# Kernel tuning notes

Measured on AMD Instinct MI355X. Metric: run time of the kernel, lower is better.

The kernel has to match this reference:

```python
import jax, jax.numpy as jnp
import numpy as np

B, T_Q, T_KV, D = 4, 2048, 4096, 1024
H = 16
HD = D // H  # head_dim = 64
EPS_LN = 1e-5
EPS_NORM = 1e-12


def setup_inputs() -> dict:
    key = jax.random.key(0)
    ks = jax.random.split(key, 12)
    inp = {
        'query': jax.random.normal(ks[0], (B, T_Q, D), jnp.float32),
        'key':   jax.random.normal(ks[1], (B, T_KV, D), jnp.float32),
        'value': jax.random.normal(ks[2], (B, T_KV, D), jnp.float32),
        # projections (nn.Linear stores weight as [out, in]; y = x @ W.T)
        'Wq': jax.random.normal(ks[3], (D, D), jnp.float32) * 0.02,
        'Wk': jax.random.normal(ks[4], (D, D), jnp.float32) * 0.02,
        'Wv': jax.random.normal(ks[5], (D, D), jnp.float32) * 0.02,
        'Wo': jax.random.normal(ks[6], (D, D), jnp.float32) * 0.01,
        'bo': jnp.zeros((D,), jnp.float32),
        'Wbeta':  jax.random.normal(ks[7], (H, D), jnp.float32) * 0.02,
        'bbeta':  jnp.zeros((H,), jnp.float32),
        'Walpha': jax.random.normal(ks[8], (H, D), jnp.float32) * 0.02,
        'balpha': jnp.full((H,), -1.0, jnp.float32),
        # per-head-dim LayerNorms
        'gq': jnp.ones((HD,), jnp.float32),
        'bq': jnp.zeros((HD,), jnp.float32),
        'gk': jnp.ones((HD,), jnp.float32),
        'bk': jnp.zeros((HD,), jnp.float32),
    }
    return inp


def _layernorm(x, g, b):
    mu = jnp.mean(x, axis=-1, keepdims=True)
    var = jnp.mean(jnp.square(x - mu), axis=-1, keepdims=True)
    return (x - mu) * jax.lax.rsqrt(var + EPS_LN) * g + b


def reference(query, key, value, Wq, Wk, Wv, Wo, bo,
              Wbeta, bbeta, Walpha, balpha, gq, bq, gk, bk):
    Bq, Tq, Dm = query.shape
    Tkv = key.shape[1]

    q = (query @ Wq.T).reshape(Bq, Tq, H, HD)
    k = (key   @ Wk.T).reshape(Bq, Tkv, H, HD)
    v = (value @ Wv.T).reshape(Bq, Tkv, H, HD)

    q = _layernorm(q, gq, bq)
    k = _layernorm(k, gk, bk)
    # F.normalize(k, dim=-1)
    k = k / jnp.maximum(jnp.linalg.norm(k, axis=-1, keepdims=True), EPS_NORM)

    beta  = jax.nn.sigmoid(key @ Wbeta.T  + bbeta)   # [B, Tkv, H]
    alpha = jax.nn.sigmoid(key @ Walpha.T + balpha)  # [B, Tkv, H]

    # time-major for scan: [Tkv, B, H, ...]
    k_t = jnp.moveaxis(k, 1, 0)
    v_t = jnp.moveaxis(v, 1, 0)
    b_t = jnp.moveaxis(beta, 1, 0)
    a_t = jnp.moveaxis(alpha, 1, 0)

    M0 = jnp.zeros((Bq, H, HD, HD), query.dtype)

    def step(M, inputs):
        kt, vt, bt, at = inputs  # [B,H,d],[B,H,d],[B,H],[B,H]
        Mk = jnp.einsum('bhij,bhj->bhi', M, kt)
        erase = at[..., None, None] * jnp.einsum('bhi,bhj->bhij', Mk, kt)
        write = bt[..., None, None] * jnp.einsum('bhi,bhj->bhij', vt, kt)
        return M - erase + write, None

    M, _ = jax.lax.scan(step, M0, (k_t, v_t, b_t, a_t))

    # out[b,t,h,i] = sum_j M[b,h,i,j] * q[b,t,h,j]
    out = jnp.einsum('bhij,bthj->bthi', M, q).reshape(Bq, Tq, Dm)
    out = out @ Wo.T + bo  # dropout is identity in eval mode
    return out
```

## Files before the change

### kernel.cpp

```cpp
#include <hip/hip_runtime.h>
#include <math.h>

#define TQ_LEN 2048
#define TKV_LEN 4096
#define BATCH 4
#define DMODEL 1024
#define NH 16
#define HD 64
#define NKBA 1152
#define CCH 128
#define NCHUNK (TKV_LEN / CCH)

typedef unsigned short u16;
typedef __attribute__((ext_vector_type(8))) short bf16x8;
typedef __attribute__((ext_vector_type(4))) float f32x4;

__device__ __forceinline__ u16 f2bf(float x) {
  union { float f; unsigned u; } c; c.f = x;
  unsigned r = c.u + 0x7fffu + ((c.u >> 16) & 1u);
  return (u16)(r >> 16);
}
__device__ __forceinline__ float bf2f(u16 x) {
  union { unsigned u; float f; } c; c.u = ((unsigned)x) << 16;
  return c.f;
}

__device__ __forceinline__ float wave_sum64(float x) {
#pragma unroll
  for (int off = 32; off; off >>= 1) x += __shfl_xor(x, off, 64);
  return x;
}

__global__ __launch_bounds__(256) void cvt_bf16_kernel(
    const float* __restrict__ s, u16* __restrict__ d) {
  size_t i = ((size_t)blockIdx.x * 256 + threadIdx.x) * 8;
  float4 a = *(const float4*)&s[i];
  float4 b = *(const float4*)&s[i + 4];
  union { u16 h[8]; uint4 v; } o;
  o.h[0] = f2bf(a.x); o.h[1] = f2bf(a.y); o.h[2] = f2bf(a.z); o.h[3] = f2bf(a.w);
  o.h[4] = f2bf(b.x); o.h[5] = f2bf(b.y); o.h[6] = f2bf(b.z); o.h[7] = f2bf(b.w);
  *(uint4*)&d[i] = o.v;
}

__global__ __launch_bounds__(256) void wcat_bf_kernel(
    const float* __restrict__ Wk, const float* __restrict__ Wb,
    const float* __restrict__ Wa, u16* __restrict__ Wcat) {
  int i = blockIdx.x * 256 + threadIdx.x;
  int row = i / DMODEL, col = i % DMODEL;
  float v;
  if (row < 1024)      v = Wk[i];
  else if (row < 1040) v = Wb[(row - 1024) * DMODEL + col];
  else if (row < 1056) v = Wa[(row - 1040) * DMODEL + col];
  else                 v = 0.f;
  Wcat[i] = f2bf(v);
}

__device__ __forceinline__ void stage_tile_bf16(
    const u16* __restrict__ G, int ldg, int row0, int kcol0,
    u16* lds, int wid, int lane) {
#pragma unroll
  for (int e = 0; e < 2; ++e) {
    int r = (wid * 2 + e) * 16;
    const u16* g = G + (size_t)(row0 + r + (lane >> 2)) * ldg + kcol0 + (lane & 3) * 8;
    __builtin_amdgcn_global_load_lds(
        (const __attribute__((address_space(1))) void*)g,
        (__attribute__((address_space(3))) void*)(lds + r * 32), 16, 0, 0);
  }
}

template <bool HAS_BIAS, bool OUT_BF16>
__global__ __launch_bounds__(256) void gemm_bt_bf16(
    const u16* __restrict__ A, const u16* __restrict__ B,
    const float* __restrict__ bias, void* __restrict__ Cv,
    int M, int N, int K, int ldc) {
  __shared__ u16 Al[2][128 * 32];
  __shared__ u16 Bl[2][128 * 32];
  const int tid = threadIdx.x;
  const int wid = tid >> 6, lane = tid & 63;
  const int wr = wid >> 1, wc = wid & 1;
  const int bm = blockIdx.y * 128, bn = blockIdx.x * 128;
  const int lrow = lane & 15, lk = (lane >> 4) * 8;

  int aoff[4], boff[4];
#pragma unroll
  for (int f = 0; f < 4; ++f) {
    aoff[f] = (wr * 64 + f * 16 + lrow) * 32 + lk;
    boff[f] = (wc * 64 + f * 16 + lrow) * 32 + lk;
  }

  f32x4 acc[4][4] = {};
  const int nk = K >> 5;
  int cur = 0;
  stage_tile_bf16(A, K, bm, 0, &Al[0][0], wid, lane);
  stage_tile_bf16(B, K, bn, 0, &Bl[0][0], wid, lane);
  __syncthreads();
  for (int kt = 0; kt < nk; ++kt) {
    if (kt + 1 < nk) {
      stage_tile_bf16(A, K, bm, (kt + 1) * 32, &Al[cur ^ 1][0], wid, lane);
      stage_tile_bf16(B, K, bn, (kt + 1) * 32, &Bl[cur ^ 1][0], wid, lane);
    }
    bf16x8 af[4], bfr[4];
#pragma unroll
    for (int f = 0; f < 4; ++f) af[f] = *(const bf16x8*)&Al[cur][aoff[f]];
#pragma unroll
    for (int f = 0; f < 4; ++f) bfr[f] = *(const bf16x8*)&Bl[cur][boff[f]];
#pragma unroll
    for (int mf = 0; mf < 4; ++mf)
#pragma unroll
      for (int nf = 0; nf < 4; ++nf)
        acc[mf][nf] = __builtin_amdgcn_mfma_f32_16x16x32_bf16(
            af[mf], bfr[nf], acc[mf][nf], 0, 0, 0);
    __syncthreads();
    cur ^= 1;
  }
  const int crow0 = bm + wr * 64 + (lane >> 4) * 4;
  const int ccol0 = bn + wc * 64 + (lane & 15);
#pragma unroll
  for (int mf = 0; mf < 4; ++mf)
#pragma unroll
    for (int nf = 0; nf < 4; ++nf) {
      int col = ccol0 + nf * 16;
      float bv = HAS_BIAS ? bias[col] : 0.f;
#pragma unroll
      for (int i = 0; i < 4; ++i) {
        int row = crow0 + mf * 16 + i;
        float vout = acc[mf][nf][i] + bv;
        if (OUT_BF16)
          ((u16*)Cv)[(size_t)row * ldc + col] = f2bf(vout);
        else
          ((float*)Cv)[(size_t)row * ldc + col] = vout;
      }
    }
}

__global__ __launch_bounds__(256) void ln_q_kernel(float* __restrict__ q,
                                                   const float* __restrict__ g,
                                                   const float* __restrict__ b) {
  int gidx = blockIdx.x * 4 + (threadIdx.x >> 6);
  int lane = threadIdx.x & 63;
  int row = gidx >> 4, h = gidx & 15;
  float* p = q + (size_t)row * DMODEL + h * HD + lane;
  float x = *p;
  float mu = wave_sum64(x) * (1.f / 64.f);
  float d = x - mu;
  float var = wave_sum64(d * d) * (1.f / 64.f);
  float y = d * rsqrtf(var + 1e-5f) * g[lane] + b[lane];
  *p = y;
}

__global__ __launch_bounds__(256) void ln_k_kernel(float* __restrict__ kb,
                                                   const float* __restrict__ g,
                                                   const float* __restrict__ b) {
  int gidx = blockIdx.x * 4 + (threadIdx.x >> 6);
  int lane = threadIdx.x & 63;
  int row = gidx >> 4, h = gidx & 15;
  float* p = kb + (size_t)row * NKBA + h * HD + lane;
  float x = *p;
  float mu = wave_sum64(x) * (1.f / 64.f);
  float d = x - mu;
  float var = wave_sum64(d * d) * (1.f / 64.f);
  float y = d * rsqrtf(var + 1e-5f) * g[lane] + b[lane];
  float s2 = wave_sum64(y * y);
  y = y / fmaxf(sqrtf(s2), 1e-12f);
  *p = y;
}

__global__ __launch_bounds__(256) void sig_kernel(
    const float* __restrict__ kb, const float* __restrict__ bb,
    const float* __restrict__ ba, float* __restrict__ beta,
    float* __restrict__ alpha) {
  int i = blockIdx.x * 256 + threadIdx.x;
  int row = i >> 4, h = i & 15;
  float lb = kb[(size_t)row * NKBA + 1024 + h] + bb[h];
  float la = kb[(size_t)row * NKBA + 1040 + h] + ba[h];
  beta[i]  = 1.f / (1.f + expf(-lb));
  alpha[i] = 1.f / (1.f + expf(-la));
}

__global__ __launch_bounds__(64, 2) void chunk_scan_kernel(
    const float* __restrict__ kb, const u16* __restrict__ v,
    const float* __restrict__ beta, const float* __restrict__ alpha,
    float* __restrict__ Pbuf, float* __restrict__ Sbuf) {
  __shared__ float klds[2][64];
  int slot = blockIdx.x;
  int bh = slot / NCHUNK, ck = slot % NCHUNK;
  int b = bh >> 4, h = bh & 15;
  int lane = threadIdx.x;
  int t0 = ck * CCH;
  const float* kbase = kb + ((size_t)b * TKV_LEN + t0) * NKBA + h * HD;
  const u16* vbase = v + ((size_t)b * TKV_LEN + t0) * DMODEL + h * HD;
  const float* bbase = beta + ((size_t)b * TKV_LEN + t0) * NH + h;
  const float* abase = alpha + ((size_t)b * TKV_LEN + t0) * NH + h;

  float P[64], S[64];
#pragma unroll
  for (int j = 0; j < 64; ++j) { P[j] = (j == lane) ? 1.f : 0.f; S[j] = 0.f; }

  klds[0][lane] = kbase[lane];
  float kn = kbase[(size_t)NKBA + lane];
  float vn = bf2f(vbase[lane]);
  float btn = bbase[0];
  float atn = abase[0];

  for (int t = 0; t < CCH; ++t) {
    float vc = vn, bt = btn, at = atn;
    if (t + 1 < CCH) {
      vn = bf2f(vbase[(size_t)(t + 1) * DMODEL + lane]);
      btn = bbase[(size_t)(t + 1) * NH];
      atn = abase[(size_t)(t + 1) * NH];
    }
    klds[(t + 1) & 1][lane] = kn;
    kn = (t + 2 < CCH) ? kbase[(size_t)(t + 2) * NKBA + lane] : 0.f;
    const float* kcur = klds[t & 1];
    float pk0 = 0.f, pk1 = 0.f, sk0 = 0.f, sk1 = 0.f;
#pragma unroll
    for (int g = 0; g < 4; ++g) {
      float4 ka = *(const float4*)&kcur[g * 16 + 0];
      float4 kc = *(const float4*)&kcur[g * 16 + 4];
      float4 ke = *(const float4*)&kcur[g * 16 + 8];
      float4 kg = *(const float4*)&kcur[g * 16 + 12];
      pk0 = fmaf(P[g*16+ 0], ka.x, pk0); pk1 = fmaf(P[g*16+ 1], ka.y, pk1);
      pk0 = fmaf(P[g*16+ 2], ka.z, pk0); pk1 = fmaf(P[g*16+ 3], ka.w, pk1);
      pk0 = fmaf(P[g*16+ 4], kc.x, pk0); pk1 = fmaf(P[g*16+ 5], kc.y, pk1);
      pk0 = fmaf(P[g*16+ 6], kc.z, pk0); pk1 = fmaf(P[g*16+ 7], kc.w, pk1);
      pk0 = fmaf(P[g*16+ 8], ke.x, pk0); pk1 = fmaf(P[g*16+ 9], ke.y, pk1);
      pk0 = fmaf(P[g*16+10], ke.z, pk0); pk1 = fmaf(P[g*16+11], ke.w, pk1);
      pk0 = fmaf(P[g*16+12], kg.x, pk0); pk1 = fmaf(P[g*16+13], kg.y, pk1);
      pk0 = fmaf(P[g*16+14], kg.z, pk0); pk1 = fmaf(P[g*16+15], kg.w, pk1);
      sk0 = fmaf(S[g*16+ 0], ka.x, sk0); sk1 = fmaf(S[g*16+ 1], ka.y, sk1);
      sk0 = fmaf(S[g*16+ 2], ka.z, sk0); sk1 = fmaf(S[g*16+ 3], ka.w, sk1);
      sk0 = fmaf(S[g*16+ 4], kc.x, sk0); sk1 = fmaf(S[g*16+ 5], kc.y, sk1);
      sk0 = fmaf(S[g*16+ 6], kc.z, sk0); sk1 = fmaf(S[g*16+ 7], kc.w, sk1);
      sk0 = fmaf(S[g*16+ 8], ke.x, sk0); sk1 = fmaf(S[g*16+ 9], ke.y, sk1);
      sk0 = fmaf(S[g*16+10], ke.z, sk0); sk1 = fmaf(S[g*16+11], ke.w, sk1);
      sk0 = fmaf(S[g*16+12], kg.x, sk0); sk1 = fmaf(S[g*16+13], kg.y, sk1);
      sk0 = fmaf(S[g*16+14], kg.z, sk0); sk1 = fmaf(S[g*16+15], kg.w, sk1);
    }
    float cp = -at * (pk0 + pk1);
    float cs = fmaf(bt, vc, -at * (sk0 + sk1));
#pragma unroll
    for (int g = 0; g < 4; ++g) {
      float4 ka = *(const float4*)&kcur[g * 16 + 0];
      float4 kc = *(const float4*)&kcur[g * 16 + 4];
      float4 ke = *(const float4*)&kcur[g * 16 + 8];
      float4 kg = *(const float4*)&kcur[g * 16 + 12];
      P[g*16+ 0] = fmaf(cp, ka.x, P[g*16+ 0]); P[g*16+ 1] = fmaf(cp, ka.y, P[g*16+ 1]);
      P[g*16+ 2] = fmaf(cp, ka.z, P[g*16+ 2]); P[g*16+ 3] = fmaf(cp, ka.w, P[g*16+ 3]);
      P[g*16+ 4] = fmaf(cp, kc.x, P[g*16+ 4]); P[g*16+ 5] = fmaf(cp, kc.y, P[g*16+ 5]);
      P[g*16+ 6] = fmaf(cp, kc.z, P[g*16+ 6]); P[g*16+ 7] = fmaf(cp, kc.w, P[g*16+ 7]);
      P[g*16+ 8] = fmaf(cp, ke.x, P[g*16+ 8]); P[g*16+ 9] = fmaf(cp, ke.y, P[g*16+ 9]);
      P[g*16+10] = fmaf(cp, ke.z, P[g*16+10]); P[g*16+11] = fmaf(cp, ke.w, P[g*16+11]);
      P[g*16+12] = fmaf(cp, kg.x, P[g*16+12]); P[g*16+13] = fmaf(cp, kg.y, P[g*16+13]);
      P[g*16+14] = fmaf(cp, kg.z, P[g*16+14]); P[g*16+15] = fmaf(cp, kg.w, P[g*16+15]);
      S[g*16+ 0] = fmaf(cs, ka.x, S[g*16+ 0]); S[g*16+ 1] = fmaf(cs, ka.y, S[g*16+ 1]);
      S[g*16+ 2] = fmaf(cs, ka.z, S[g*16+ 2]); S[g*16+ 3] = fmaf(cs, ka.w, S[g*16+ 3]);
      S[g*16+ 4] = fmaf(cs, kc.x, S[g*16+ 4]); S[g*16+ 5] = fmaf(cs, kc.y, S[g*16+ 5]);
      S[g*16+ 6] = fmaf(cs, kc.z, S[g*16+ 6]); S[g*16+ 7] = fmaf(cs, kc.w, S[g*16+ 7]);
      S[g*16+ 8] = fmaf(cs, ke.x, S[g*16+ 8]); S[g*16+ 9] = fmaf(cs, ke.y, S[g*16+ 9]);
      S[g*16+10] = fmaf(cs, ke.z, S[g*16+10]); S[g*16+11] = fmaf(cs, ke.w, S[g*16+11]);
      S[g*16+12] = fmaf(cs, kg.x, S[g*16+12]); S[g*16+13] = fmaf(cs, kg.y, S[g*16+13]);
      S[g*16+14] = fmaf(cs, kg.z, S[g*16+14]); S[g*16+15] = fmaf(cs, kg.w, S[g*16+15]);
    }
  }
  float* po = Pbuf + (size_t)slot * 4096 + (size_t)lane * 64;
  float* so = Sbuf + (size_t)slot * 4096 + (size_t)lane * 64;
#pragma unroll
  for (int j4 = 0; j4 < 16; ++j4) {
    *(float4*)&po[j4 * 4] = make_float4(P[4 * j4], P[4 * j4 + 1], P[4 * j4 + 2], P[4 * j4 + 3]);
    *(float4*)&so[j4 * 4] = make_float4(S[4 * j4], S[4 * j4 + 1], S[4 * j4 + 2], S[4 * j4 + 3]);
  }
}

__global__ __launch_bounds__(256) void fold_kernel(
    const float* __restrict__ Pin, const float* __restrict__ Sin,
    float* __restrict__ Pout, float* __restrict__ Sout, int nitems) {
  __shared__ float Pa[64][68], Sa[64][68], Pc[64][68], Sc[64][68];
  const int tid = threadIdx.x;
  const int r0 = (tid >> 4) * 4, c0 = (tid & 15) * 4;
  for (int l = tid; l < 4096; l += 256) {
    int r = l >> 6, c = l & 63;
    Pa[r][c] = (r == c) ? 1.f : 0.f;
    Sa[r][c] = 0.f;
  }
  for (int item = 0; item < nitems; ++item) {
    const float* pg = Pin + ((size_t)blockIdx.x * nitems + item) * 4096;
    const float* sg = Sin + ((size_t)blockIdx.x * nitems + item) * 4096;
#pragma unroll
    for (int e = 0; e < 4; ++e) {
      int l = tid * 16 + e * 4;
      int r = l >> 6, c = l & 63;
      *(float4*)&Pc[r][c] = *(const float4*)&pg[l];
      *(float4*)&Sc[r][c] = *(const float4*)&sg[l];
    }
    __syncthreads();
    float accP[4][4] = {}, accS[4][4] = {};
#pragma unroll 4
    for (int j4 = 0; j4 < 16; ++j4) {
      float bmat[4][4];
#pragma unroll
      for (int jj = 0; jj < 4; ++jj) {
        float4 t = *(const float4*)&Pc[j4 * 4 + jj][c0];
        bmat[jj][0] = t.x; bmat[jj][1] = t.y; bmat[jj][2] = t.z; bmat[jj][3] = t.w;
      }
#pragma unroll
      for (int rr = 0; rr < 4; ++rr) {
        float4 tp = *(const float4*)&Pa[r0 + rr][j4 * 4];
        float4 ts = *(const float4*)&Sa[r0 + rr][j4 * 4];
        float ap[4] = {tp.x, tp.y, tp.z, tp.w};
        float as[4] = {ts.x, ts.y, ts.z, ts.w};
#pragma unroll
        for (int jj = 0; jj < 4; ++jj)
#pragma unroll
          for (int cc = 0; cc < 4; ++cc) {
            accP[rr][cc] = fmaf(ap[jj], bmat[jj][cc], accP[rr][cc]);
            accS[rr][cc] = fmaf(as[jj], bmat[jj][cc], accS[rr][cc]);
          }
      }
    }
#pragma unroll
    for (int rr = 0; rr < 4; ++rr)
#pragma unroll
      for (int cc = 0; cc < 4; ++cc) accS[rr][cc] += Sc[r0 + rr][c0 + cc];
    __syncthreads();
#pragma unroll
    for (int rr = 0; rr < 4; ++rr)
#pragma unroll
      for (int cc = 0; cc < 4; ++cc) {
        Pa[r0 + rr][c0 + cc] = accP[rr][cc];
        Sa[r0 + rr][c0 + cc] = accS[rr][cc];
      }
  }
  __syncthreads();
  float* po = Pout + (size_t)blockIdx.x * 4096;
  float* so = Sout + (size_t)blockIdx.x * 4096;
#pragma unroll
  for (int e = 0; e < 4; ++e) {
    int l = tid * 16 + e * 4;
    int r = l >> 6, c = l & 63;
    *(float4*)&po[l] = *(const float4*)&Pa[r][c];
    *(float4*)&so[l] = *(const float4*)&Sa[r][c];
  }
}

__global__ __launch_bounds__(256) void outm_kernel(
    const float* __restrict__ Mg, const float* __restrict__ q,
    u16* __restrict__ attn) {
  __shared__ float Ml[64][65];
  int bh = blockIdx.x;
  int tchunk = blockIdx.y;
  int b = bh >> 4, h = bh & 15;
  int tid = threadIdx.x;
  const float* mg = Mg + (size_t)bh * 4096;
#pragma unroll
  for (int e = 0; e < 16; ++e) {
    int l = tid + e * 256;
    Ml[l >> 6][l & 63] = mg[l];
  }
  __syncthreads();
  int lane = tid & 63, tt = tid >> 6;
  const float* qb = q + ((size_t)b * TQ_LEN + tchunk * 256) * DMODEL + h * HD;
  u16* ob = attn + ((size_t)b * TQ_LEN + tchunk * 256) * DMODEL + h * HD;
  for (int it = 0; it < 64; ++it) {
    int t = it * 4 + tt;
    const float* qr = qb + (size_t)t * DMODEL;
    float acc = 0.f;
#pragma unroll
    for (int j4 = 0; j4 < 16; ++j4) {
      float4 qv = *(const float4*)&qr[j4 * 4];
      acc += Ml[lane][j4 * 4 + 0] * qv.x + Ml[lane][j4 * 4 + 1] * qv.y +
             Ml[lane][j4 * 4 + 2] * qv.z + Ml[lane][j4 * 4 + 3] * qv.w;
    }
    ob[(size_t)t * DMODEL + lane] = f2bf(acc);
  }
}

extern "C" void kernel_launch(void* const* d_in, const int* in_sizes, int n_in,
                              void* d_out, int out_size, void* d_ws,
                              size_t ws_size, hipStream_t stream) {
  const float* query = (const float*)d_in[0];
  const float* key   = (const float*)d_in[1];
  const float* value = (const float*)d_in[2];
  const float* Wq    = (const float*)d_in[3];
  const float* Wk    = (const float*)d_in[4];
  const float* Wv    = (const float*)d_in[5];
  const float* Wo    = (const float*)d_in[6];
  const float* bo    = (const float*)d_in[7];
  const float* Wbeta = (const float*)d_in[8];
  const float* bbeta = (const float*)d_in[9];
  const float* Walpha= (const float*)d_in[10];
  const float* balpha= (const float*)d_in[11];
  const float* gq    = (const float*)d_in[12];
  const float* bq    = (const float*)d_in[13];
  const float* gk    = (const float*)d_in[14];
  const float* bk    = (const float*)d_in[15];
  float* out = (float*)d_out;

  const int MQ = BATCH * TQ_LEN;
  const int MKV = BATCH * TKV_LEN;
  const int NSLOT = 64 * NCHUNK;

  float* ws = (float*)d_ws;
  size_t off = 0;
  u16* Wcat_bf = (u16*)(ws + off); off += (size_t)NKBA * DMODEL / 2;
  u16* Wq_bf   = (u16*)(ws + off); off += (size_t)DMODEL * DMODEL / 2;
  u16* Wv_bf   = (u16*)(ws + off); off += (size_t)DMODEL * DMODEL / 2;
  u16* Wo_bf   = (u16*)(ws + off); off += (size_t)DMODEL * DMODEL / 2;
  u16* qbf = (u16*)(ws + off); size_t qbf_f = off; off += (size_t)MQ * DMODEL / 2;
  u16* kbf = (u16*)(ws + off); size_t kbf_f = off; off += (size_t)MKV * DMODEL / 2;
  u16* vbf = (u16*)(ws + off); size_t vbf_f = off; off += (size_t)MKV * DMODEL / 2;
  float* qp   = ws + off; off += (size_t)MQ * DMODEL;
  float* kba  = ws + off; size_t kba_f = off; off += (size_t)MKV * NKBA;
  u16* vpb = (u16*)(ws + off); off += (size_t)MKV * DMODEL / 2;
  float* Pbuf = ws + kbf_f;
  float* Sbuf = ws + vbf_f;
  float* Gp   = ws + qbf_f;
  float* Gs   = ws + qbf_f + 1048576;
  float* Fp   = ws + qbf_f + 2097152;
  float* beta = ws + qbf_f + 2359296;
  float* alpha= ws + qbf_f + 2621440;
  float* Mg   = ws + qbf_f + 2883584;
  u16* attn_bf = (u16*)(ws + kba_f);

  wcat_bf_kernel<<<NKBA * DMODEL / 256, 256, 0, stream>>>(Wk, Wbeta, Walpha, Wcat_bf);
  cvt_bf16_kernel<<<DMODEL * DMODEL / 2048, 256, 0, stream>>>(Wq, Wq_bf);
  cvt_bf16_kernel<<<DMODEL * DMODEL / 2048, 256, 0, stream>>>(Wv, Wv_bf);
  cvt_bf16_kernel<<<DMODEL * DMODEL / 2048, 256, 0, stream>>>(Wo, Wo_bf);
  cvt_bf16_kernel<<<MQ * DMODEL / 2048, 256, 0, stream>>>(query, qbf);
  cvt_bf16_kernel<<<MKV * DMODEL / 2048, 256, 0, stream>>>(key, kbf);
  cvt_bf16_kernel<<<MKV * DMODEL / 2048, 256, 0, stream>>>(value, vbf);
  gemm_bt_bf16<false, false><<<dim3(DMODEL / 128, MQ / 128), 256, 0, stream>>>(
      qbf, Wq_bf, nullptr, qp, MQ, DMODEL, DMODEL, DMODEL);
  gemm_bt_bf16<false, false><<<dim3(NKBA / 128, MKV / 128), 256, 0, stream>>>(
      kbf, Wcat_bf, nullptr, kba, MKV, NKBA, DMODEL, NKBA);
  gemm_bt_bf16<false, true><<<dim3(DMODEL / 128, MKV / 128), 256, 0, stream>>>(
      vbf, Wv_bf, nullptr, vpb, MKV, DMODEL, DMODEL, DMODEL);
  ln_q_kernel<<<MQ * NH / 4, 256, 0, stream>>>(qp, gq, bq);
  ln_k_kernel<<<MKV * NH / 4, 256, 0, stream>>>(kba, gk, bk);
  sig_kernel<<<MKV * NH / 256, 256, 0, stream>>>(kba, bbeta, balpha, beta, alpha);
  chunk_scan_kernel<<<NSLOT, 64, 0, stream>>>(kba, vpb, beta, alpha, Pbuf, Sbuf);
  fold_kernel<<<NSLOT / 8, 256, 0, stream>>>(Pbuf, Sbuf, Gp, Gs, 8);
  fold_kernel<<<64, 256, 0, stream>>>(Gp, Gs, Fp, Mg, 4);
  outm_kernel<<<dim3(64, TQ_LEN / 256), 256, 0, stream>>>(Mg, qp, attn_bf);
  gemm_bt_bf16<true, false><<<dim3(DMODEL / 128, MQ / 128), 256, 0, stream>>>(
      attn_bf, Wo_bf, bo, out, MQ, DMODEL, DMODEL, DMODEL);
  (void)in_sizes; (void)n_in; (void)out_size; (void)ws_size;
}
```

Measured before the change: 606.6 us.

## Replace 128x128 GEMM with 256x256 tile, 8-wave ping-pong pipelined GEMM

Swaps the 128x128, K=32 double-buffered bf16 GEMM for a 256x256, K=64 tile kernel with 512 threads. The new kernel interleaves global-to-LDS staging with MFMA phases using explicit barriers, wave priority and vmcnt waits, and adds an XCD-aware block swizzle. NKBA is padded to 1280 so the concatenated K/beta/alpha projection divides into 256-wide tiles. The aim is more data reuse per LDS byte and better overlap of memory with compute, at the cost of 128 KB of LDS, fewer blocks (smaller grids), and some wasted compute on the padded columns.

```diff
diff --git a/kernel.cpp b/kernel.cpp
--- a/kernel.cpp
+++ b/kernel.cpp
@@ -7,7 +7,7 @@
 #define DMODEL 1024
 #define NH 16
 #define HD 64
-#define NKBA 1152
+#define NKBA 1280
 #define CCH 128
 #define NCHUNK (TKV_LEN / CCH)
 
@@ -55,82 +55,138 @@
   Wcat[i] = f2bf(v);
 }
 
-__device__ __forceinline__ void stage_tile_bf16(
-    const u16* __restrict__ G, int ldg, int row0, int kcol0,
-    u16* lds, int wid, int lane) {
+#define BAR() __builtin_amdgcn_s_barrier()
+#define PRIO(x) __builtin_amdgcn_s_setprio(x)
+#define VMCNT(n)                                              \
+  do {                                                        \
+    __builtin_amdgcn_sched_barrier(0);                        \
+    asm volatile("s_waitcnt vmcnt(" #n ")" ::: "memory");     \
+  } while (0)
+
+__device__ __forceinline__ void stage_half256(
+    const u16* __restrict__ G, int ldg, int row0, int kc, int h,
+    u16* ldsmat, int wid, int lane) {
 #pragma unroll
   for (int e = 0; e < 2; ++e) {
-    int r = (wid * 2 + e) * 16;
-    const u16* g = G + (size_t)(row0 + r + (lane >> 2)) * ldg + kcol0 + (lane & 3) * 8;
+    int j0 = wid * 64 + e * 512;
+    int j = j0 + lane;
+    int r = h * 128 + (j >> 3);
+    int cg = (j & 7) * 8;
+    const u16* g = G + (size_t)(row0 + r) * ldg + kc + cg;
     __builtin_amdgcn_global_load_lds(
         (const __attribute__((address_space(1))) void*)g,
-        (__attribute__((address_space(3))) void*)(lds + r * 32), 16, 0, 0);
-  }
-}
+        (__attribute__((address_space(3))) void*)(ldsmat + h * 8192 + j0 * 8),
+        16, 0, 0);
+  }
+}
+
+#define READ_A(L, h_)                                                         \
+  do {                                                                        \
+    _Pragma("unroll") for (int mf = 0; mf < 4; ++mf)                          \
+    _Pragma("unroll") for (int kk = 0; kk < 2; ++kk)                          \
+      af[mf][kk] = *(const bf16x8*)&(L)[(wm * 128 + (h_) * 64 + mf * 16 +     \
+                                         lrow) * 64 + kk * 32 + lk8];         \
+  } while (0)
+
+#define READ_B(L, n_, dst)                                                    \
+  do {                                                                        \
+    _Pragma("unroll") for (int nf = 0; nf < 2; ++nf)                          \
+    _Pragma("unroll") for (int kk = 0; kk < 2; ++kk)                          \
+      dst[nf][kk] = *(const bf16x8*)&(L)[(wn * 64 + (n_) * 32 + nf * 16 +     \
+                                          lrow) * 64 + kk * 32 + lk8];        \
+  } while (0)
+
+#define MFMA_Q(h_, n_, bfx)                                                   \
+  do {                                                                        \
+    _Pragma("unroll") for (int mf = 0; mf < 4; ++mf)                          \
+    _Pragma("unroll") for (int nf = 0; nf < 2; ++nf)                          \
+    _Pragma("unroll") for (int kk = 0; kk < 2; ++kk)                          \
+      acc[h_][mf][n_][nf] = __builtin_amdgcn_mfma_f32_16x16x32_bf16(          \
+          af[mf][kk], bfx[nf][kk], acc[h_][mf][n_][nf], 0, 0, 0);             \
+  } while (0)
 
 template <bool HAS_BIAS, bool OUT_BF16>
-__global__ __launch_bounds__(256) void gemm_bt_bf16(
+__global__ __launch_bounds__(512, 2) void gemm_bt_256(
     const u16* __restrict__ A, const u16* __restrict__ B,
     const float* __restrict__ bias, void* __restrict__ Cv,
-    int M, int N, int K, int ldc) {
-  __shared__ u16 Al[2][128 * 32];
-  __shared__ u16 Bl[2][128 * 32];
+    int K, int ldc, int nbx) {
+  __shared__ u16 lds[2][2][16384];
   const int tid = threadIdx.x;
-  const int wid = tid >> 6, lane = tid & 63;
-  const int wr = wid >> 1, wc = wid & 1;
-  const int bm = blockIdx.y * 128, bn = blockIdx.x * 128;
-  const int lrow = lane & 15, lk = (lane >> 4) * 8;
-
-  int aoff[4], boff[4];
-#pragma unroll
-  for (int f = 0; f < 4; ++f) {
-    aoff[f] = (wr * 64 + f * 16 + lrow) * 32 + lk;
-    boff[f] = (wc * 64 + f * 16 + lrow) * 32 + lk;
-  }
-
-  f32x4 acc[4][4] = {};
-  const int nk = K >> 5;
-  int cur = 0;
-  stage_tile_bf16(A, K, bm, 0, &Al[0][0], wid, lane);
-  stage_tile_bf16(B, K, bn, 0, &Bl[0][0], wid, lane);
-  __syncthreads();
-  for (int kt = 0; kt < nk; ++kt) {
-    if (kt + 1 < nk) {
-      stage_tile_bf16(A, K, bm, (kt + 1) * 32, &Al[cur ^ 1][0], wid, lane);
-      stage_tile_bf16(B, K, bn, (kt + 1) * 32, &Bl[cur ^ 1][0], wid, lane);
-    }
-    bf16x8 af[4], bfr[4];
-#pragma unroll
-    for (int f = 0; f < 4; ++f) af[f] = *(const bf16x8*)&Al[cur][aoff[f]];
-#pragma unroll
-    for (int f = 0; f < 4; ++f) bfr[f] = *(const bf16x8*)&Bl[cur][boff[f]];
-#pragma unroll
-    for (int mf = 0; mf < 4; ++mf)
-#pragma unroll
-      for (int nf = 0; nf < 4; ++nf)
-        acc[mf][nf] = __builtin_amdgcn_mfma_f32_16x16x32_bf16(
-            af[mf], bfr[nf], acc[mf][nf], 0, 0, 0);
-    __syncthreads();
-    cur ^= 1;
-  }
-  const int crow0 = bm + wr * 64 + (lane >> 4) * 4;
-  const int ccol0 = bn + wc * 64 + (lane & 15);
-#pragma unroll
-  for (int mf = 0; mf < 4; ++mf)
-#pragma unroll
-    for (int nf = 0; nf < 4; ++nf) {
-      int col = ccol0 + nf * 16;
-      float bv = HAS_BIAS ? bias[col] : 0.f;
-#pragma unroll
-      for (int i = 0; i < 4; ++i) {
-        int row = crow0 + mf * 16 + i;
-        float vout = acc[mf][nf][i] + bv;
-        if (OUT_BF16)
-          ((u16*)Cv)[(size_t)row * ldc + col] = f2bf(vout);
-        else
-          ((float*)Cv)[(size_t)row * ldc + col] = vout;
-      }
-    }
+  const int lane = tid & 63, wid = tid >> 6;
+  const int wm = wid >> 2, wn = wid & 3;
+  const int nwg = gridDim.x, cpx = nwg >> 3, orig = blockIdx.x;
+  const int swz = (orig & 7) * cpx + (orig >> 3);
+  const int bm = (swz / nbx) * 256, bn = (swz % nbx) * 256;
+  const int lrow = lane & 15, lk8 = (lane >> 4) * 8;
+  const int NT = K >> 6;
+
+  f32x4 acc[2][4][2][2] = {};
+  bf16x8 af[4][2], bf0[2][2], bf1[2][2];
+
+  u16* lA0 = &lds[0][0][0]; u16* lB0 = &lds[0][1][0];
+  u16* lA1 = &lds[1][0][0]; u16* lB1 = &lds[1][1][0];
+
+  stage_half256(A, K, bm, 0, 0, lA0, wid, lane);
+  stage_half256(A, K, bm, 0, 1, lA0, wid, lane);
+  stage_half256(B, K, bn, 0, 0, lB0, wid, lane);
+  stage_half256(B, K, bn, 0, 1, lB0, wid, lane);
+  stage_half256(B, K, bn, 64, 0, lB1, wid, lane);
+  stage_half256(B, K, bn, 64, 1, lB1, wid, lane);
+  VMCNT(0);
+  BAR();
+
+  for (int i = 0; i < NT / 2; ++i) {
+    const int t0 = 2 * i, t1 = 2 * i + 1;
+    READ_A(lA0, 0);
+    READ_B(lB0, 0, bf0);
+    stage_half256(A, K, bm, t1 * 64, 0, lA1, wid, lane);
+    BAR(); PRIO(1); MFMA_Q(0, 0, bf0); PRIO(0); BAR();
+    READ_B(lB0, 1, bf1);
+    stage_half256(A, K, bm, t1 * 64, 1, lA1, wid, lane);
+    BAR(); PRIO(1); MFMA_Q(0, 1, bf1); PRIO(0); BAR();
+    READ_A(lA0, 1);
+    if (t0 + 2 < NT) stage_half256(B, K, bn, (t0 + 2) * 64, 0, lB0, wid, lane);
+    BAR(); PRIO(1); MFMA_Q(1, 0, bf0); PRIO(0); BAR();
+    if (t0 + 2 < NT) stage_half256(B, K, bn, (t0 + 2) * 64, 1, lB0, wid, lane);
+    BAR(); PRIO(1); MFMA_Q(1, 1, bf1); PRIO(0);
+    VMCNT(4);
+    BAR();
+    READ_A(lA1, 0);
+    READ_B(lB1, 0, bf0);
+    if (t0 + 2 < NT) stage_half256(A, K, bm, (t0 + 2) * 64, 0, lA0, wid, lane);
+    BAR(); PRIO(1); MFMA_Q(0, 0, bf0); PRIO(0); BAR();
+    READ_B(lB1, 1, bf1);
+    if (t0 + 2 < NT) stage_half256(A, K, bm, (t0 + 2) * 64, 1, lA0, wid, lane);
+    BAR(); PRIO(1); MFMA_Q(0, 1, bf1); PRIO(0); BAR();
+    READ_A(lA1, 1);
+    if (t1 + 2 < NT) stage_half256(B, K, bn, (t1 + 2) * 64, 0, lB1, wid, lane);
+    BAR(); PRIO(1); MFMA_Q(1, 0, bf0); PRIO(0); BAR();
+    if (t1 + 2 < NT) stage_half256(B, K, bn, (t1 + 2) * 64, 1, lB1, wid, lane);
+    BAR(); PRIO(1); MFMA_Q(1, 1, bf1); PRIO(0);
+    VMCNT(4);
+    BAR();
+  }
+
+#pragma unroll
+  for (int h = 0; h < 2; ++h)
+#pragma unroll
+    for (int n = 0; n < 2; ++n)
+#pragma unroll
+      for (int mf = 0; mf < 4; ++mf)
+#pragma unroll
+        for (int nf = 0; nf < 2; ++nf) {
+          int col = bn + wn * 64 + n * 32 + nf * 16 + (lane & 15);
+          float bv = HAS_BIAS ? bias[col] : 0.f;
+          int row0 = bm + wm * 128 + h * 64 + mf * 16 + (lane >> 4) * 4;
+#pragma unroll
+          for (int ii = 0; ii < 4; ++ii) {
+            float vout = acc[h][mf][n][nf][ii] + bv;
+            if (OUT_BF16)
+              ((u16*)Cv)[(size_t)(row0 + ii) * ldc + col] = f2bf(vout);
+            else
+              ((float*)Cv)[(size_t)(row0 + ii) * ldc + col] = vout;
+          }
+        }
 }
 
 __global__ __launch_bounds__(256) void ln_q_kernel(float* __restrict__ q,
@@ -428,12 +484,12 @@
   cvt_bf16_kernel<<<MQ * DMODEL / 2048, 256, 0, stream>>>(query, qbf);
   cvt_bf16_kernel<<<MKV * DMODEL / 2048, 256, 0, stream>>>(key, kbf);
   cvt_bf16_kernel<<<MKV * DMODEL / 2048, 256, 0, stream>>>(value, vbf);
-  gemm_bt_bf16<false, false><<<dim3(DMODEL / 128, MQ / 128), 256, 0, stream>>>(
-      qbf, Wq_bf, nullptr, qp, MQ, DMODEL, DMODEL, DMODEL);
-  gemm_bt_bf16<false, false><<<dim3(NKBA / 128, MKV / 128), 256, 0, stream>>>(
-      kbf, Wcat_bf, nullptr, kba, MKV, NKBA, DMODEL, NKBA);
-  gemm_bt_bf16<false, true><<<dim3(DMODEL / 128, MKV / 128), 256, 0, stream>>>(
-      vbf, Wv_bf, nullptr, vpb, MKV, DMODEL, DMODEL, DMODEL);
+  gemm_bt_256<false, false><<<(DMODEL / 256) * (MQ / 256), 512, 0, stream>>>(
+      qbf, Wq_bf, nullptr, qp, DMODEL, DMODEL, DMODEL / 256);
+  gemm_bt_256<false, false><<<(NKBA / 256) * (MKV / 256), 512, 0, stream>>>(
+      kbf, Wcat_bf, nullptr, kba, DMODEL, NKBA, NKBA / 256);
+  gemm_bt_256<false, true><<<(DMODEL / 256) * (MKV / 256), 512, 0, stream>>>(
+      vbf, Wv_bf, nullptr, vpb, DMODEL, DMODEL, DMODEL / 256);
   ln_q_kernel<<<MQ * NH / 4, 256, 0, stream>>>(qp, gq, bq);
   ln_k_kernel<<<MKV * NH / 4, 256, 0, stream>>>(kba, gk, bk);
   sig_kernel<<<MKV * NH / 256, 256, 0, stream>>>(kba, bbeta, balpha, beta, alpha);
@@ -441,7 +497,7 @@
   fold_kernel<<<NSLOT / 8, 256, 0, stream>>>(Pbuf, Sbuf, Gp, Gs, 8);
   fold_kernel<<<64, 256, 0, stream>>>(Gp, Gs, Fp, Mg, 4);
   outm_kernel<<<dim3(64, TQ_LEN / 256), 256, 0, stream>>>(Mg, qp, attn_bf);
-  gemm_bt_bf16<true, false><<<dim3(DMODEL / 128, MQ / 128), 256, 0, stream>>>(
-      attn_bf, Wo_bf, bo, out, MQ, DMODEL, DMODEL, DMODEL);
+  gemm_bt_256<true, false><<<(DMODEL / 256) * (MQ / 256), 512, 0, stream>>>(
+      attn_bf, Wo_bf, bo, out, DMODEL, DMODEL, DMODEL / 256);
   (void)in_sizes; (void)n_in; (void)out_size; (void)ws_size;
 }
```

Measured after the change: 632.9 us. +4.3%, slower.
